# Optimization experiments

Measured on AMD Instinct MI355X. Metric: run time of the kernel, lower is better.

The kernel has to match this reference:

```python
import jax, jax.numpy as jnp
import numpy as np

N_HEAD = 16


def setup_inputs() -> dict:
    key = jax.random.key(0)
    ks = jax.random.split(key, 5)
    B, T, D_IN, D = 2, 2048, 1152, 1024
    s_in = 1.0 / np.sqrt(D_IN)
    s_d = 1.0 / np.sqrt(D)
    return {
        "xp": jax.random.normal(ks[0], (B, T, D_IN), jnp.float32),
        "Wq": jax.random.normal(ks[1], (D_IN, D), jnp.float32) * s_in,
        "bq": jnp.zeros((D,), jnp.float32),
        "Wk": jax.random.normal(ks[2], (D_IN, D), jnp.float32) * s_in,
        "bk": jnp.zeros((D,), jnp.float32),
        "Wv": jax.random.normal(ks[3], (D_IN, D), jnp.float32) * s_in,
        "bv": jnp.zeros((D,), jnp.float32),
        "Wp": jax.random.normal(ks[4], (D, D), jnp.float32) * s_d,
        "bp": jnp.zeros((D,), jnp.float32),
    }


def reference(xp, Wq, bq, Wk, bk, Wv, bv, Wp, bp):
    B, T, _ = xp.shape
    D = Wq.shape[1]
    hd = D // N_HEAD  # head dim
    # q, k, v projections -> [B, H, T, hd]
    def split_heads(t):
        return t.reshape(B, T, N_HEAD, hd).transpose(0, 2, 1, 3)
    q = split_heads(xp @ Wq + bq)
    k = split_heads(xp @ Wk + bk)
    v = split_heads(xp @ Wv + bv)
    scale = 1.0 / np.sqrt(hd).astype(np.float32)
    att = jnp.einsum("bhqd,bhkd->bhqk", q, k) * scale  # [B,H,T,T]
    causal = jnp.tril(jnp.ones((T, T), bool))
    att = jnp.where(causal[None, None], att, -jnp.inf)
    att = jax.nn.softmax(att, axis=-1)
    y = jnp.einsum("bhqk,bhkd->bhqd", att, v)  # [B,H,T,hd]
    y = y.transpose(0, 2, 1, 3).reshape(B, T, D)
    return y @ Wp + bp
```

## Files before the change

kernel.cpp:

```cpp
#include <hip/hip_runtime.h>
#include <hip/hip_bf16.h>

typedef __attribute__((ext_vector_type(8))) short bf16x8;
typedef __attribute__((ext_vector_type(4))) float f32x4;
typedef __attribute__((ext_vector_type(16))) float f32x16;

__device__ __forceinline__ void gload_lds16(const void* g, void* l) {
    __builtin_amdgcn_global_load_lds(
        (const __attribute__((address_space(1))) unsigned int*)g,
        (__attribute__((address_space(3))) unsigned int*)l, 16, 0, 0);
}

__device__ __forceinline__ unsigned int pk2(float x, float y) {
    union { __hip_bfloat16 h[2]; unsigned int u; } z;
    z.h[0] = __float2bfloat16(x); z.h[1] = __float2bfloat16(y);
    return z.u;
}

__global__ void k_cvt_bf16(const float* __restrict__ x, __hip_bfloat16* __restrict__ o, int n8) {
    int i = blockIdx.x * 256 + threadIdx.x;
    if (i >= n8) return;
    const float4* xp = (const float4*)(x + (size_t)i * 8);
    float4 a = xp[0], b = xp[1];
    union { __hip_bfloat16 h[8]; uint4 u; } tu;
    tu.h[0] = __float2bfloat16(a.x); tu.h[1] = __float2bfloat16(a.y);
    tu.h[2] = __float2bfloat16(a.z); tu.h[3] = __float2bfloat16(a.w);
    tu.h[4] = __float2bfloat16(b.x); tu.h[5] = __float2bfloat16(b.y);
    tu.h[6] = __float2bfloat16(b.z); tu.h[7] = __float2bfloat16(b.w);
    *(uint4*)(o + (size_t)i * 8) = tu.u;
}

__global__ void k_tr3(const float* __restrict__ s0, const float* __restrict__ s1,
                      const float* __restrict__ s2, __hip_bfloat16* __restrict__ dst,
                      int K, int N) {
    __shared__ float tile[32][33];
    const float* src = (blockIdx.z == 0) ? s0 : ((blockIdx.z == 1) ? s1 : s2);
    __hip_bfloat16* d = dst + (size_t)blockIdx.z * N * K;
    int n0 = blockIdx.x * 32, k0 = blockIdx.y * 32;
    int tx = threadIdx.x & 31, ty = threadIdx.x >> 5;
#pragma unroll
    for (int i = 0; i < 4; i++)
        tile[ty + i * 8][tx] = src[(size_t)(k0 + ty + i * 8) * N + n0 + tx];
    __syncthreads();
#pragma unroll
    for (int i = 0; i < 4; i++)
        d[(size_t)(n0 + ty + i * 8) * K + k0 + tx] = __float2bfloat16(tile[tx][ty + i * 8]);
}

__global__ void k_tr(const float* __restrict__ src, __hip_bfloat16* __restrict__ dst, int K, int N) {
    __shared__ float tile[32][33];
    int n0 = blockIdx.x * 32, k0 = blockIdx.y * 32;
    int tx = threadIdx.x & 31, ty = threadIdx.x >> 5;
#pragma unroll
    for (int i = 0; i < 4; i++)
        tile[ty + i * 8][tx] = src[(size_t)(k0 + ty + i * 8) * N + n0 + tx];
    __syncthreads();
#pragma unroll
    for (int i = 0; i < 4; i++)
        dst[(size_t)(n0 + ty + i * 8) * K + k0 + tx] = __float2bfloat16(tile[tx][ty + i * 8]);
}

#define QSCALE 0.18033688011111204f

template <int EPI>
__global__ __launch_bounds__(256, 2) void k_gemm(
    const __hip_bfloat16* __restrict__ A, const __hip_bfloat16* __restrict__ Bt,
    int M, int N, int K,
    const float* __restrict__ b0, const float* __restrict__ b1, const float* __restrict__ b2,
    __hip_bfloat16* __restrict__ qb, __hip_bfloat16* __restrict__ kb, __hip_bfloat16* __restrict__ vb,
    float* __restrict__ outp)
{
    __shared__ __align__(16) __hip_bfloat16 As[128 * 64];
    __shared__ __align__(16) __hip_bfloat16 Bs[128 * 64];
    const int t = threadIdx.x;
    const int lane = t & 63, w = t >> 6;
    const int wr = w >> 1, wc = w & 1;
    const int r16 = lane & 15, kg = lane >> 4;
    const int m0 = blockIdx.x * 128, n0 = blockIdx.y * 128;
    f32x4 acc[4][4] = {};
    const int ksteps = K >> 6;
    for (int kt = 0; kt < ksteps; ++kt) {
        if (kt) __syncthreads();
        const int ks = kt * 64;
#pragma unroll
        for (int i = 0; i < 4; i++) {
            int ci = i * 256 + t;
            int row = ci >> 3, kc = (ci & 7) * 8;
            gload_lds16(A + (size_t)(m0 + row) * K + ks + kc, As + ci * 8);
        }
#pragma unroll
        for (int i = 0; i < 4; i++) {
            int ci = i * 256 + t;
            int row = ci >> 3, kc = (ci & 7) * 8;
            gload_lds16(Bt + (size_t)(n0 + row) * K + ks + kc, Bs + ci * 8);
        }
        __syncthreads();
#pragma unroll
        for (int c = 0; c < 2; c++) {
            bf16x8 af[4], bfr[4];
#pragma unroll
            for (int mi = 0; mi < 4; mi++)
                af[mi] = *(const bf16x8*)(As + (wr * 64 + mi * 16 + r16) * 64 + c * 32 + kg * 8);
#pragma unroll
            for (int ni = 0; ni < 4; ni++)
                bfr[ni] = *(const bf16x8*)(Bs + (wc * 64 + ni * 16 + r16) * 64 + c * 32 + kg * 8);
#pragma unroll
            for (int mi = 0; mi < 4; mi++)
#pragma unroll
                for (int ni = 0; ni < 4; ni++)
                    acc[mi][ni] = __builtin_amdgcn_mfma_f32_16x16x32_bf16(af[mi], bfr[ni], acc[mi][ni], 0, 0, 0);
        }
    }
#pragma unroll
    for (int mi = 0; mi < 4; mi++) {
#pragma unroll
        for (int ni = 0; ni < 4; ni++) {
#pragma unroll
            for (int j = 0; j < 4; j++) {
                int m = m0 + wr * 64 + mi * 16 + kg * 4 + j;
                int n = n0 + wc * 64 + ni * 16 + r16;
                float val = acc[mi][ni][j];
                if (EPI == 0) {
                    int proj = n >> 10, r = n & 1023;
                    int hh = r >> 6, dd = r & 63;
                    int bb = m >> 11, tt = m & 2047;
                    if (proj == 0) {
                        val = (val + b0[r]) * QSCALE;
                        qb[((size_t)(bb * 16 + hh) * 2048 + tt) * 64 + dd] = __float2bfloat16(val);
                    } else if (proj == 1) {
                        val += b1[r];
                        kb[((size_t)(bb * 16 + hh) * 2048 + tt) * 64 + dd] = __float2bfloat16(val);
                    } else {
                        val += b2[r];
                        vb[((size_t)(bb * 16 + hh) * 64 + dd) * 2048 + tt] = __float2bfloat16(val);
                    }
                } else {
                    outp[(size_t)m * N + n] = val + b0[n];
                }
            }
        }
    }
}

__global__ __launch_bounds__(256, 2) void k_attn(
    const __hip_bfloat16* __restrict__ qbuf,
    const __hip_bfloat16* __restrict__ kbuf,
    const __hip_bfloat16* __restrict__ vtbuf,
    __hip_bfloat16* __restrict__ y)
{
    __shared__ __align__(16) __hip_bfloat16 Kl[3][64 * 64];
    __shared__ __align__(16) __hip_bfloat16 Vl[3][64 * 64];
    const int t = threadIdx.x, lane = t & 63, w = t >> 6;
    const int l31 = lane & 31, hi = lane >> 5;
    const int g = blockIdx.x;
    const int c2 = g >> 8, p = g & 255;
    const int bh = p & 31;
    const int rr = p >> 5;
    const int qt = c2 ? (15 - rr) : rr;
    const int nt = 2 * qt + 2;
    const int q0w = qt * 128 + w * 32;
    const int swr = (l31 & 7) << 3;

    const __hip_bfloat16* qp = qbuf + ((size_t)bh * 2048 + q0w + l31) * 64;
    bf16x8 qf[4];
#pragma unroll
    for (int dt = 0; dt < 4; dt++)
        qf[dt] = *(const bf16x8*)(qp + dt * 16 + hi * 8);

    f32x16 O0 = {}, O1 = {};
    float m_s = -3.0e38f, l_s = 0.f;
    const __hip_bfloat16* kb = kbuf + (size_t)bh * 2048 * 64;
    const __hip_bfloat16* vb = vtbuf + (size_t)bh * 64 * 2048;

    const int ci0 = t, ci1 = 256 + t;
    const int kr0 = ci0 >> 3, sc0 = ((ci0 & 7) * 8) ^ ((kr0 & 7) << 3);
    const int kr1 = ci1 >> 3, sc1 = ((ci1 & 7) * 8) ^ ((kr1 & 7) << 3);

#pragma unroll
    for (int pt = 0; pt < 2; ++pt) {
        gload_lds16(kb + (size_t)pt * 4096 + (size_t)kr0 * 64 + sc0, &Kl[pt][ci0 * 8]);
        gload_lds16(kb + (size_t)pt * 4096 + (size_t)kr1 * 64 + sc1, &Kl[pt][ci1 * 8]);
        gload_lds16(vb + (size_t)kr0 * 2048 + pt * 64 + sc0, &Vl[pt][ci0 * 8]);
        gload_lds16(vb + (size_t)kr1 * 2048 + pt * 64 + sc1, &Vl[pt][ci1 * 8]);
    }

    for (int kt = 0; kt < nt; ++kt) {
        if (kt < nt - 1) {
            asm volatile("s_waitcnt vmcnt(4)" ::: "memory");
        } else {
            asm volatile("s_waitcnt vmcnt(0)" ::: "memory");
        }
        __builtin_amdgcn_s_barrier();
        __builtin_amdgcn_sched_barrier(0);
        if (kt + 2 < nt) {
            const int kn = kt + 2;
            const int nb = kn % 3;
            gload_lds16(kb + (size_t)kn * 4096 + (size_t)kr0 * 64 + sc0, &Kl[nb][ci0 * 8]);
            gload_lds16(kb + (size_t)kn * 4096 + (size_t)kr1 * 64 + sc1, &Kl[nb][ci1 * 8]);
            gload_lds16(vb + (size_t)kr0 * 2048 + kn * 64 + sc0, &Vl[nb][ci0 * 8]);
            gload_lds16(vb + (size_t)kr1 * 2048 + kn * 64 + sc1, &Vl[nb][ci1 * 8]);
        }
        const int cb = kt % 3;
        const int kbase = kt * 64;
        if (kbase <= q0w + 31) {
            const __hip_bfloat16* Klb = Kl[cb];
            const __hip_bfloat16* Vlb = Vl[cb];
            f32x16 s0 = {}, s1 = {};
#pragma unroll
            for (int dt = 0; dt < 4; dt++) {
                bf16x8 ka = *(const bf16x8*)(Klb + l31 * 64 + ((dt * 16 + hi * 8) ^ swr));
                s0 = __builtin_amdgcn_mfma_f32_32x32x16_bf16(ka, qf[dt], s0, 0, 0, 0);
            }
#pragma unroll
            for (int dt = 0; dt < 4; dt++) {
                bf16x8 kb2 = *(const bf16x8*)(Klb + (32 + l31) * 64 + ((dt * 16 + hi * 8) ^ swr));
                s1 = __builtin_amdgcn_mfma_f32_32x32x16_bf16(kb2, qf[dt], s1, 0, 0, 0);
            }
            if (kbase + 63 > q0w) {
                const int qg = q0w + l31;
#pragma unroll
                for (int r = 0; r < 16; ++r) {
                    const int krow = (r & 3) + 8 * (r >> 2) + 4 * hi;
                    if (kbase + krow > qg) s0[r] = -3.0e38f;
                    if (kbase + 32 + krow > qg) s1[r] = -3.0e38f;
                }
            }
            float rmax = s0[0];
#pragma unroll
            for (int r = 1; r < 16; ++r) rmax = fmaxf(rmax, s0[r]);
#pragma unroll
            for (int r = 0; r < 16; ++r) rmax = fmaxf(rmax, s1[r]);
            rmax = fmaxf(rmax, __shfl_xor(rmax, 32));
            if (__any(rmax > m_s + 8.0f)) {
                const float mn = fmaxf(m_s, rmax);
                const float al = exp2f(m_s - mn);
                m_s = mn;
                l_s *= al;
#pragma unroll
                for (int r = 0; r < 16; ++r) {
                    const int qrow = (r & 3) + 8 * (r >> 2) + 4 * hi;
                    const float ar = __shfl(al, qrow);
                    O0[r] *= ar; O1[r] *= ar;
                }
            }
            float rsum = 0.f;
#pragma unroll
            for (int r = 0; r < 16; ++r) { s0[r] = exp2f(s0[r] - m_s); rsum += s0[r]; }
#pragma unroll
            for (int r = 0; r < 16; ++r) { s1[r] = exp2f(s1[r] - m_s); rsum += s1[r]; }
            rsum += __shfl_xor(rsum, 32);
            l_s += rsum;
            bf16x8 pa[4];
#pragma unroll
            for (int kt4 = 0; kt4 < 4; ++kt4) {
                const f32x16& sc = (kt4 < 2) ? s0 : s1;
                const int a8 = (kt4 & 1) * 8;
                const unsigned int plo0 = pk2(sc[a8 + 0], sc[a8 + 1]);
                const unsigned int plo1 = pk2(sc[a8 + 2], sc[a8 + 3]);
                const unsigned int phi0 = pk2(sc[a8 + 4], sc[a8 + 5]);
                const unsigned int phi1 = pk2(sc[a8 + 6], sc[a8 + 7]);
                const unsigned int snd0 = hi ? plo0 : phi0;
                const unsigned int snd1 = hi ? plo1 : phi1;
                const unsigned int r0 = (unsigned int)__shfl_xor((int)snd0, 32);
                const unsigned int r1 = (unsigned int)__shfl_xor((int)snd1, 32);
                union { unsigned int u[4]; bf16x8 v; } fr;
                fr.u[0] = hi ? r0 : plo0;
                fr.u[1] = hi ? r1 : plo1;
                fr.u[2] = hi ? phi0 : r0;
                fr.u[3] = hi ? phi1 : r1;
                pa[kt4] = fr.v;
            }
#pragma unroll
            for (int kt4 = 0; kt4 < 4; ++kt4) {
                bf16x8 vf0 = *(const bf16x8*)(Vlb + l31 * 64 + ((kt4 * 16 + hi * 8) ^ swr));
                O0 = __builtin_amdgcn_mfma_f32_32x32x16_bf16(pa[kt4], vf0, O0, 0, 0, 0);
                bf16x8 vf1 = *(const bf16x8*)(Vlb + (32 + l31) * 64 + ((kt4 * 16 + hi * 8) ^ swr));
                O1 = __builtin_amdgcn_mfma_f32_32x32x16_bf16(pa[kt4], vf1, O1, 0, 0, 0);
            }
        }
    }
    const int b = bh >> 4, h = bh & 15;
    const float linv = 1.0f / l_s;
#pragma unroll
    for (int r = 0; r < 16; ++r) {
        const int qrow = (r & 3) + 8 * (r >> 2) + 4 * hi;
        const float iv = __shfl(linv, qrow);
        const size_t ro = ((size_t)b * 2048 + q0w + qrow) * 1024 + (size_t)h * 64;
        y[ro + l31] = __float2bfloat16(O0[r] * iv);
        y[ro + 32 + l31] = __float2bfloat16(O1[r] * iv);
    }
}

extern "C" void kernel_launch(void* const* d_in, const int* in_sizes, int n_in,
                              void* d_out, int out_size, void* d_ws, size_t ws_size,
                              hipStream_t stream) {
    const float* xp = (const float*)d_in[0];
    const float* Wq = (const float*)d_in[1];
    const float* bq = (const float*)d_in[2];
    const float* Wk = (const float*)d_in[3];
    const float* bk = (const float*)d_in[4];
    const float* Wv = (const float*)d_in[5];
    const float* bv = (const float*)d_in[6];
    const float* Wp = (const float*)d_in[7];
    const float* bp = (const float*)d_in[8];
    float* out = (float*)d_out;

    char* ws = (char*)d_ws;
    __hip_bfloat16* xb     = (__hip_bfloat16*)(ws);
    __hip_bfloat16* Wqkv_t = (__hip_bfloat16*)(ws + 9437184);
    __hip_bfloat16* Wp_t   = (__hip_bfloat16*)(ws + 16515072);
    __hip_bfloat16* qb     = (__hip_bfloat16*)(ws + 18612224);
    __hip_bfloat16* kbv    = (__hip_bfloat16*)(ws + 27000832);
    __hip_bfloat16* vtb    = (__hip_bfloat16*)(ws + 35389440);
    __hip_bfloat16* yb     = (__hip_bfloat16*)(ws + 43778048);

    k_cvt_bf16<<<2304, 256, 0, stream>>>(xp, xb, 589824);
    dim3 trg3(1024 / 32, 1152 / 32, 3);
    k_tr3<<<trg3, 256, 0, stream>>>(Wq, Wk, Wv, Wqkv_t, 1152, 1024);
    dim3 trg2(1024 / 32, 1024 / 32);
    k_tr<<<trg2, 256, 0, stream>>>(Wp, Wp_t, 1024, 1024);

    dim3 g1(4096 / 128, 3072 / 128);
    k_gemm<0><<<g1, 256, 0, stream>>>(xb, Wqkv_t, 4096, 3072, 1152, bq, bk, bv, qb, kbv, vtb, nullptr);
    k_attn<<<512, 256, 0, stream>>>(qb, kbv, vtb, yb);
    dim3 g2(4096 / 128, 1024 / 128);
    k_gemm<1><<<g2, 256, 0, stream>>>(yb, Wp_t, 4096, 1024, 1024, bp, nullptr, nullptr,
                                      nullptr, nullptr, nullptr, out);
}
```

Measured before the change: 151.0 us.

## Split attention into 64-row query tiles with 2-wave blocks and double buffering

The attention kernel now runs 1024 blocks of 128 threads, each covering a 64-row query tile, instead of 512 blocks of 256 threads covering 128 rows. The grid mapping is remapped so heavy and light causal tiles are interleaved. The K/V staging drops from a three-buffer asynchronous pipeline to a two-buffer scheme with __syncthreads, which cuts LDS use per block. It also adds s_setprio around the MFMA sections and uses tree reductions for the row max and row sum. The aim is better load balance and occupancy, at the cost of more K/V reloads per head and a full barrier on every iteration.

```diff
diff --git a/kernel.cpp b/kernel.cpp
--- a/kernel.cpp
+++ b/kernel.cpp
@@ -142,23 +142,23 @@
     }
 }
 
-__global__ __launch_bounds__(256, 2) void k_attn(
+__global__ __launch_bounds__(128, 2) void k_attn(
     const __hip_bfloat16* __restrict__ qbuf,
     const __hip_bfloat16* __restrict__ kbuf,
     const __hip_bfloat16* __restrict__ vtbuf,
     __hip_bfloat16* __restrict__ y)
 {
-    __shared__ __align__(16) __hip_bfloat16 Kl[3][64 * 64];
-    __shared__ __align__(16) __hip_bfloat16 Vl[3][64 * 64];
+    __shared__ __align__(16) __hip_bfloat16 Kl[2][64 * 64];
+    __shared__ __align__(16) __hip_bfloat16 Vl[2][64 * 64];
     const int t = threadIdx.x, lane = t & 63, w = t >> 6;
     const int l31 = lane & 31, hi = lane >> 5;
     const int g = blockIdx.x;
-    const int c2 = g >> 8, p = g & 255;
-    const int bh = p & 31;
-    const int rr = p >> 5;
-    const int qt = c2 ? (15 - rr) : rr;
-    const int nt = 2 * qt + 2;
-    const int q0w = qt * 128 + w * 32;
+    const int c4 = g >> 8, p = g & 255;
+    const int bh = (p >> 5) * 4 + c4;
+    const int rr = p & 31;
+    const int qt = (c4 & 1) ? rr : 31 - rr;
+    const int nt = qt + 1;
+    const int q0w = qt * 64 + w * 32;
     const int swr = (l31 & 7) << 3;
 
     const __hip_bfloat16* qp = qbuf + ((size_t)bh * 2048 + q0w + l31) * 64;
@@ -172,40 +172,35 @@
     const __hip_bfloat16* kb = kbuf + (size_t)bh * 2048 * 64;
     const __hip_bfloat16* vb = vtbuf + (size_t)bh * 64 * 2048;
 
-    const int ci0 = t, ci1 = 256 + t;
-    const int kr0 = ci0 >> 3, sc0 = ((ci0 & 7) * 8) ^ ((kr0 & 7) << 3);
-    const int kr1 = ci1 >> 3, sc1 = ((ci1 & 7) * 8) ^ ((kr1 & 7) << 3);
-
-#pragma unroll
-    for (int pt = 0; pt < 2; ++pt) {
-        gload_lds16(kb + (size_t)pt * 4096 + (size_t)kr0 * 64 + sc0, &Kl[pt][ci0 * 8]);
-        gload_lds16(kb + (size_t)pt * 4096 + (size_t)kr1 * 64 + sc1, &Kl[pt][ci1 * 8]);
-        gload_lds16(vb + (size_t)kr0 * 2048 + pt * 64 + sc0, &Vl[pt][ci0 * 8]);
-        gload_lds16(vb + (size_t)kr1 * 2048 + pt * 64 + sc1, &Vl[pt][ci1 * 8]);
-    }
+    int krw[4], scl[4];
+#pragma unroll
+    for (int c = 0; c < 4; c++) {
+        const int ci = c * 128 + t;
+        krw[c] = ci >> 3;
+        scl[c] = ((ci & 7) * 8) ^ ((krw[c] & 7) << 3);
+    }
+
+    auto stage = [&](int buf, int kt) {
+#pragma unroll
+        for (int c = 0; c < 4; c++)
+            gload_lds16(kb + ((size_t)kt * 64 + krw[c]) * 64 + scl[c], &Kl[buf][(c * 128 + t) * 8]);
+#pragma unroll
+        for (int c = 0; c < 4; c++)
+            gload_lds16(vb + (size_t)krw[c] * 2048 + kt * 64 + scl[c], &Vl[buf][(c * 128 + t) * 8]);
+    };
+
+    stage(0, 0);
+    __syncthreads();
 
     for (int kt = 0; kt < nt; ++kt) {
-        if (kt < nt - 1) {
-            asm volatile("s_waitcnt vmcnt(4)" ::: "memory");
-        } else {
-            asm volatile("s_waitcnt vmcnt(0)" ::: "memory");
-        }
-        __builtin_amdgcn_s_barrier();
-        __builtin_amdgcn_sched_barrier(0);
-        if (kt + 2 < nt) {
-            const int kn = kt + 2;
-            const int nb = kn % 3;
-            gload_lds16(kb + (size_t)kn * 4096 + (size_t)kr0 * 64 + sc0, &Kl[nb][ci0 * 8]);
-            gload_lds16(kb + (size_t)kn * 4096 + (size_t)kr1 * 64 + sc1, &Kl[nb][ci1 * 8]);
-            gload_lds16(vb + (size_t)kr0 * 2048 + kn * 64 + sc0, &Vl[nb][ci0 * 8]);
-            gload_lds16(vb + (size_t)kr1 * 2048 + kn * 64 + sc1, &Vl[nb][ci1 * 8]);
-        }
-        const int cb = kt % 3;
+        const int cur = kt & 1;
+        if (kt + 1 < nt) stage(cur ^ 1, kt + 1);
         const int kbase = kt * 64;
         if (kbase <= q0w + 31) {
-            const __hip_bfloat16* Klb = Kl[cb];
-            const __hip_bfloat16* Vlb = Vl[cb];
+            const __hip_bfloat16* Klb = Kl[cur];
+            const __hip_bfloat16* Vlb = Vl[cur];
             f32x16 s0 = {}, s1 = {};
+            __builtin_amdgcn_s_setprio(1);
 #pragma unroll
             for (int dt = 0; dt < 4; dt++) {
                 bf16x8 ka = *(const bf16x8*)(Klb + l31 * 64 + ((dt * 16 + hi * 8) ^ swr));
@@ -216,6 +211,7 @@
                 bf16x8 kb2 = *(const bf16x8*)(Klb + (32 + l31) * 64 + ((dt * 16 + hi * 8) ^ swr));
                 s1 = __builtin_amdgcn_mfma_f32_32x32x16_bf16(kb2, qf[dt], s1, 0, 0, 0);
             }
+            __builtin_amdgcn_s_setprio(0);
             if (kbase + 63 > q0w) {
                 const int qg = q0w + l31;
 #pragma unroll
@@ -225,12 +221,14 @@
                     if (kbase + 32 + krow > qg) s1[r] = -3.0e38f;
                 }
             }
-            float rmax = s0[0];
-#pragma unroll
-            for (int r = 1; r < 16; ++r) rmax = fmaxf(rmax, s0[r]);
-#pragma unroll
-            for (int r = 0; r < 16; ++r) rmax = fmaxf(rmax, s1[r]);
-            rmax = fmaxf(rmax, __shfl_xor(rmax, 32));
+            float a[16];
+#pragma unroll
+            for (int r = 0; r < 16; ++r) a[r] = fmaxf(s0[r], s1[r]);
+#pragma unroll
+            for (int s = 8; s > 0; s >>= 1)
+#pragma unroll
+                for (int r = 0; r < s; ++r) a[r] = fmaxf(a[r], a[r + s]);
+            float rmax = fmaxf(a[0], __shfl_xor(a[0], 32));
             if (__any(rmax > m_s + 8.0f)) {
                 const float mn = fmaxf(m_s, rmax);
                 const float al = exp2f(m_s - mn);
@@ -243,13 +241,16 @@
                     O0[r] *= ar; O1[r] *= ar;
                 }
             }
-            float rsum = 0.f;
-#pragma unroll
-            for (int r = 0; r < 16; ++r) { s0[r] = exp2f(s0[r] - m_s); rsum += s0[r]; }
-#pragma unroll
-            for (int r = 0; r < 16; ++r) { s1[r] = exp2f(s1[r] - m_s); rsum += s1[r]; }
-            rsum += __shfl_xor(rsum, 32);
-            l_s += rsum;
+#pragma unroll
+            for (int r = 0; r < 16; ++r) { s0[r] = exp2f(s0[r] - m_s); s1[r] = exp2f(s1[r] - m_s); }
+            float b2[16];
+#pragma unroll
+            for (int r = 0; r < 16; ++r) b2[r] = s0[r] + s1[r];
+#pragma unroll
+            for (int s = 8; s > 0; s >>= 1)
+#pragma unroll
+                for (int r = 0; r < s; ++r) b2[r] += b2[r + s];
+            l_s += b2[0] + __shfl_xor(b2[0], 32);
             bf16x8 pa[4];
 #pragma unroll
             for (int kt4 = 0; kt4 < 4; ++kt4) {
@@ -270,6 +271,7 @@
                 fr.u[3] = hi ? phi1 : r1;
                 pa[kt4] = fr.v;
             }
+            __builtin_amdgcn_s_setprio(1);
 #pragma unroll
             for (int kt4 = 0; kt4 < 4; ++kt4) {
                 bf16x8 vf0 = *(const bf16x8*)(Vlb + l31 * 64 + ((kt4 * 16 + hi * 8) ^ swr));
@@ -277,7 +279,9 @@
                 bf16x8 vf1 = *(const bf16x8*)(Vlb + (32 + l31) * 64 + ((kt4 * 16 + hi * 8) ^ swr));
                 O1 = __builtin_amdgcn_mfma_f32_32x32x16_bf16(pa[kt4], vf1, O1, 0, 0, 0);
             }
-        }
+            __builtin_amdgcn_s_setprio(0);
+        }
+        __syncthreads();
     }
     const int b = bh >> 4, h = bh & 15;
     const float linv = 1.0f / l_s;
@@ -322,7 +326,7 @@
 
     dim3 g1(4096 / 128, 3072 / 128);
     k_gemm<0><<<g1, 256, 0, stream>>>(xb, Wqkv_t, 4096, 3072, 1152, bq, bk, bv, qb, kbv, vtb, nullptr);
-    k_attn<<<512, 256, 0, stream>>>(qb, kbv, vtb, yb);
+    k_attn<<<1024, 128, 0, stream>>>(qb, kbv, vtb, yb);
     dim3 g2(4096 / 128, 1024 / 128);
     k_gemm<1><<<g2, 256, 0, stream>>>(yb, Wp_t, 4096, 1024, 1024, bp, nullptr, nullptr,
                                       nullptr, nullptr, nullptr, out);
```

Result: slower. 154.1 us (+2.0%).
